# Performance work log

Measured on AMD Instinct MI355X. Metric: run time of the kernel, lower is better.

The kernel has to match this reference:

```python
import jax, jax.numpy as jnp
import numpy as np

N_GRAPHS = 32
NODES_PER_GRAPH = 512
N = N_GRAPHS * NODES_PER_GRAPH
DEG = 32
E = N * DEG
D = 128
HID = 256
NEXP = 8
EHID = 64
L = 3
CUTOFF = 10.0
ROUTE_W = 0.1


def _graph_norm(x, seg, w, b, ms, num, eps=1e-5):
    # PyG GraphNorm: x - mean_scale*mean_per_graph, normalized by per-graph std
    cnt = jax.ops.segment_sum(jnp.ones((x.shape[0],), x.dtype), seg, num_segments=num)[:, None]
    mean = jax.ops.segment_sum(x, seg, num_segments=num) / cnt
    out = x - ms * mean[seg]
    var = jax.ops.segment_sum(out * out, seg, num_segments=num) / cnt
    std = jnp.sqrt(var + eps)
    return w * out / std[seg] + b


def setup_inputs() -> dict:
    key = jax.random.key(0)
    ks = jax.random.split(key, 8)
    rng = np.random.default_rng(0)
    # radius-graph surrogate: each node gathers DEG in-graph neighbors
    tgt = np.repeat(np.arange(N), DEG)
    src = (tgt // NODES_PER_GRAPH) * NODES_PER_GRAPH + rng.integers(0, NODES_PER_GRAPH, size=E)
    edge_index = jnp.asarray(np.stack([src, tgt]), dtype=jnp.int32)
    batch = jnp.asarray(np.arange(N) // NODES_PER_GRAPH, dtype=jnp.int32)
    atom_type = jax.random.randint(ks[0], (N,), 0, 200, dtype=jnp.int32)
    pos = jax.random.uniform(ks[1], (N, 3), jnp.float32) * 5.0  # box side 5 -> dist < CUTOFF
    s = 0.1
    emb = jax.random.normal(ks[2], (200, D), jnp.float32) * s
    edge_w1 = jax.random.normal(ks[3], (L, 1, EHID), jnp.float32) * s
    edge_b1 = jnp.zeros((L, EHID), jnp.float32)
    edge_w2 = jax.random.normal(ks[4], (L, EHID, NEXP), jnp.float32) * s
    edge_b2 = jnp.zeros((L, NEXP), jnp.float32)
    node_w1 = jax.random.normal(ks[5], (L, NEXP, D, HID), jnp.float32) * s
    node_b1 = jnp.zeros((L, NEXP, HID), jnp.float32)
    node_w2 = jax.random.normal(ks[6], (L, NEXP, HID, D), jnp.float32) * s
    node_b2 = jnp.zeros((L, NEXP, D), jnp.float32)
    gn_w = jnp.ones((L, D), jnp.float32)
    gn_b = jnp.zeros((L, D), jnp.float32)
    gn_ms = jnp.ones((L, D), jnp.float32)
    dn_w = jnp.ones((1,), jnp.float32)
    dn_b = jnp.zeros((1,), jnp.float32)
    dn_ms = jnp.ones((1,), jnp.float32)
    return dict(pos=pos, emb=emb, edge_w1=edge_w1, edge_b1=edge_b1, edge_w2=edge_w2, edge_b2=edge_b2,
                node_w1=node_w1, node_b1=node_b1, node_w2=node_w2, node_b2=node_b2,
                gn_w=gn_w, gn_b=gn_b, gn_ms=gn_ms, dn_w=dn_w, dn_b=dn_b, dn_ms=dn_ms,
                atom_type=atom_type, edge_index=edge_index, batch=batch)


def reference(pos, emb, edge_w1, edge_b1, edge_w2, edge_b2, node_w1, node_b1, node_w2, node_b2,
              gn_w, gn_b, gn_ms, dn_w, dn_b, dn_ms, atom_type, edge_index, batch):
    src, dst = edge_index[0], edge_index[1]  # message j -> i
    dist = jnp.sqrt(jnp.sum((pos[src] - pos[dst]) ** 2, axis=-1))  # [E]
    ebatch = batch[src]
    edge_attr0 = _graph_norm(dist[:, None], ebatch, dn_w, dn_b, dn_ms, N_GRAPHS)  # [E,1]
    ew = (CUTOFF - dist[:, None]) / CUTOFF  # [E,1]
    h = emb[atom_type]  # [N,D]
    total_lbl = jnp.float32(0.0)
    for l in range(L):
        hid_e = jnp.maximum(edge_attr0 @ edge_w1[l] + edge_b1[l], 0.0)  # [E,EHID]
        ea = jax.nn.softmax(hid_e @ edge_w2[l] + edge_b2[l], axis=-1)  # [E,NEXP]
        total_lbl = total_lbl + jnp.sum(jnp.mean(ea, axis=0) ** 2) * NEXP / L
        eaw = ea * ew  # [E,NEXP] routing weight * distance weight
        x_j = h[src]  # [E,D] gathered once per layer
        out = jnp.zeros((N, D), h.dtype)
        for e in range(NEXP):
            agg = jax.ops.segment_sum(x_j * eaw[:, e:e + 1], dst, num_segments=N)  # [N,D]
            h2 = jnp.maximum(agg @ node_w1[l, e] + node_b1[l, e], 0.0) @ node_w2[l, e] + node_b2[l, e]
            out = out + h2
        h = out
        if l + 1 < L:
            h = jnp.tanh(_graph_norm(h, batch, gn_w[l], gn_b[l], gn_ms[l], N_GRAPHS))
    cnt = jax.ops.segment_sum(jnp.ones((N,), h.dtype), batch, num_segments=N_GRAPHS)[:, None]
    pooled = (jax.ops.segment_sum(h, batch, num_segments=N_GRAPHS) / cnt).mean(-1)  # [G]
    return pooled, total_lbl * ROUTE_W
```

## Files before the change

kernel.cpp:

```cpp
#include <hip/hip_runtime.h>
#include <math.h>

#define NG    32
#define NPG   512
#define NN    16384
#define DEG   32
#define NE    524288
#define EPG   16384
#define DD    128
#define HIDN  256
#define NEXPT 8
#define EHID  64
#define NL    3

typedef __attribute__((ext_vector_type(8))) short bh8;
typedef __attribute__((ext_vector_type(4))) float f4;

__device__ __forceinline__ unsigned short bf16_1(float x) {
  unsigned int u = __float_as_uint(x);
  return (unsigned short)((u + 0x7fffu + ((u >> 16) & 1u)) >> 16);
}
__device__ __forceinline__ unsigned int bf16pair(float a, float b) {
  return (unsigned int)bf16_1(a) | ((unsigned int)bf16_1(b) << 16);
}

__global__ void k_zero(float4* p, int n4) {
  int i = blockIdx.x * 256 + threadIdx.x;
  if (i < n4) p[i] = make_float4(0.f, 0.f, 0.f, 0.f);
}

__global__ void k_tr(const float* __restrict__ in, unsigned short* __restrict__ outp,
                     int M, int N) {
  __shared__ float tile[32][33];
  const float* ip = in + (size_t)blockIdx.z * M * N;
  unsigned short* op = outp + (size_t)blockIdx.z * M * N;
  int t = threadIdx.x;
  int i = t >> 5, j = t & 31;
  int c0 = blockIdx.x * 32, r0 = blockIdx.y * 32;
#pragma unroll
  for (int p = 0; p < 4; ++p)
    tile[i + 8 * p][j] = ip[(size_t)(r0 + i + 8 * p) * N + c0 + j];
  __syncthreads();
#pragma unroll
  for (int p = 0; p < 4; ++p)
    op[(size_t)(c0 + i + 8 * p) * M + r0 + j] = bf16_1(tile[j][i + 8 * p]);
}

__global__ void k_dist(const float* __restrict__ pos, const int* __restrict__ src,
                       const int* __restrict__ dst, float* __restrict__ dist,
                       float* __restrict__ gsum, float* __restrict__ gsq) {
  int e = blockIdx.x * 256 + threadIdx.x;
  int s = src[e], t = dst[e];
  float dx = pos[3 * s]     - pos[3 * t];
  float dy = pos[3 * s + 1] - pos[3 * t + 1];
  float dz = pos[3 * s + 2] - pos[3 * t + 2];
  float d = sqrtf(dx * dx + dy * dy + dz * dz);
  dist[e] = d;
  float s1 = d, s2 = d * d;
  for (int o = 32; o; o >>= 1) { s1 += __shfl_down(s1, o); s2 += __shfl_down(s2, o); }
  __shared__ float r1[4], r2[4];
  int w = threadIdx.x >> 6;
  if ((threadIdx.x & 63) == 0) { r1[w] = s1; r2[w] = s2; }
  __syncthreads();
  if (threadIdx.x == 0) {
    int g = e >> 14;
    atomicAdd(&gsum[g], r1[0] + r1[1] + r1[2] + r1[3]);
    atomicAdd(&gsq[g],  r2[0] + r2[1] + r2[2] + r2[3]);
  }
}

__global__ void k_efin(const float* __restrict__ gsum, const float* __restrict__ gsq,
                       const float* __restrict__ dnw, const float* __restrict__ dnb,
                       const float* __restrict__ dnms, float* __restrict__ ga, float* __restrict__ gb) {
  int g = threadIdx.x;
  if (g < NG) {
    float ms = dnms[0];
    float mean = gsum[g] * (1.f / EPG);
    float var = gsq[g] * (1.f / EPG) - (2.f * ms - ms * ms) * mean * mean;
    float a = dnw[0] * rsqrtf(var + 1e-5f);
    ga[g] = a;
    gb[g] = dnb[0] - a * ms * mean;
  }
}

__global__ void k_embed(const float4* __restrict__ emb, const int* __restrict__ at,
                        float4* __restrict__ h) {
  int gid = blockIdx.x * 256 + threadIdx.x;
  int i = gid >> 5, q = gid & 31;
  h[gid] = emb[at[i] * 32 + q];
}

__global__ void k_edge(const float* __restrict__ dist,
                       const float* __restrict__ ga, const float* __restrict__ gb,
                       const float* __restrict__ ew1, const float* __restrict__ eb1,
                       const float* __restrict__ ew2, const float* __restrict__ eb2,
                       float* __restrict__ eaw, float* __restrict__ part) {
  __shared__ float w1s[EHID], b1s[EHID];
  __shared__ __align__(16) float w2s[EHID * NEXPT];
  __shared__ float b2s[NEXPT];
  int t = threadIdx.x;
  if (t < EHID) { w1s[t] = ew1[t]; b1s[t] = eb1[t]; }
  if (t < NEXPT) b2s[t] = eb2[t];
  for (int j = t; j < EHID * NEXPT; j += 256) w2s[j] = ew2[j];
  __syncthreads();

  int e0 = blockIdx.x * 1024 + t * 4;
  float4 dv = *(const float4*)&dist[e0];
  float dd[4] = {dv.x, dv.y, dv.z, dv.w};
  int g = e0 >> 14;
  float gav = ga[g], gbv = gb[g];
  float a0[4], ewv[4];
#pragma unroll
  for (int j = 0; j < 4; ++j) {
    a0[j] = gav * dd[j] + gbv;
    ewv[j] = (10.0f - dd[j]) * 0.1f;
  }
  float acc[4][NEXPT];
#pragma unroll
  for (int j = 0; j < 4; ++j)
#pragma unroll
    for (int x = 0; x < NEXPT; ++x) acc[j][x] = b2s[x];

  for (int k = 0; k < EHID; ++k) {
    float w1k = w1s[k], b1k = b1s[k];
    float hk[4];
#pragma unroll
    for (int j = 0; j < 4; ++j) hk[j] = fmaxf(a0[j] * w1k + b1k, 0.f);
    float4 wa = *(const float4*)&w2s[k * 8];
    float4 wb = *(const float4*)&w2s[k * 8 + 4];
    float ww[8] = {wa.x, wa.y, wa.z, wa.w, wb.x, wb.y, wb.z, wb.w};
#pragma unroll
    for (int j = 0; j < 4; ++j)
#pragma unroll
      for (int x = 0; x < NEXPT; ++x) acc[j][x] += hk[j] * ww[x];
  }

  float esum[NEXPT] = {0, 0, 0, 0, 0, 0, 0, 0};
#pragma unroll
  for (int j = 0; j < 4; ++j) {
    float m = acc[j][0];
#pragma unroll
    for (int x = 1; x < NEXPT; ++x) m = fmaxf(m, acc[j][x]);
    float p[NEXPT], s = 0.f;
#pragma unroll
    for (int x = 0; x < NEXPT; ++x) { p[x] = __expf(acc[j][x] - m); s += p[x]; }
    float inv = 1.f / s;
    float fw = ewv[j] * inv;
    float4 o0 = {p[0] * fw, p[1] * fw, p[2] * fw, p[3] * fw};
    float4 o1 = {p[4] * fw, p[5] * fw, p[6] * fw, p[7] * fw};
    *(float4*)&eaw[(size_t)(e0 + j) * 8]     = o0;
    *(float4*)&eaw[(size_t)(e0 + j) * 8 + 4] = o1;
#pragma unroll
    for (int x = 0; x < NEXPT; ++x) esum[x] += p[x] * inv;
  }
  for (int o = 32; o; o >>= 1)
#pragma unroll
    for (int x = 0; x < NEXPT; ++x) esum[x] += __shfl_down(esum[x], o);
  __shared__ float ps[4][NEXPT];
  int w = t >> 6;
  if ((t & 63) == 0)
#pragma unroll
    for (int x = 0; x < NEXPT; ++x) ps[w][x] = esum[x];
  __syncthreads();
  if (t < NEXPT) part[blockIdx.x * NEXPT + t] = ps[0][t] + ps[1][t] + ps[2][t] + ps[3][t];
}

__global__ __launch_bounds__(256) void k_agg(const float* __restrict__ h, const int* __restrict__ src,
                      const float* __restrict__ eaw, unsigned short* __restrict__ agg) {
  const int t = threadIdx.x;
  const int s = t >> 5;
  const int lane = t & 31;
  const int i = blockIdx.x * 8 + s;
  __shared__ int ssrc[8][DEG];
  __shared__ __align__(16) float sw[8][DEG][NEXPT];
  const int e0b = blockIdx.x * 8 * DEG;
  ssrc[s][lane] = src[e0b + t];
  {
    const float4* ep = (const float4*)&eaw[(size_t)e0b * 8];
    float4* sp = (float4*)&sw[0][0][0];
    sp[t] = ep[t];
    sp[t + 256] = ep[t + 256];
  }
  __syncthreads();
  f4 acc[NEXPT];
#pragma unroll
  for (int x = 0; x < NEXPT; ++x) acc[x] = (f4)0.f;
#pragma unroll 2
  for (int k = 0; k < DEG; ++k) {
    f4 hv = *(const f4*)&h[(size_t)ssrc[s][k] * 128 + lane * 4];
    f4 w0 = *(const f4*)&sw[s][k][0];
    f4 w1 = *(const f4*)&sw[s][k][4];
    float ww[8] = {w0[0], w0[1], w0[2], w0[3], w1[0], w1[1], w1[2], w1[3]};
#pragma unroll
    for (int x = 0; x < NEXPT; ++x) acc[x] += ww[x] * hv;
  }
#pragma unroll
  for (int x = 0; x < NEXPT; ++x) {
    uint2 pk;
    pk.x = bf16pair(acc[x][0], acc[x][1]);
    pk.y = bf16pair(acc[x][2], acc[x][3]);
    *(uint2*)&agg[((size_t)x * NN + i) * 128 + lane * 4] = pk;
  }
}

__global__ __launch_bounds__(256) void k_mlp(
    const unsigned short* __restrict__ agg,
    const unsigned short* __restrict__ w1t,
    const float* __restrict__ b1g,
    const unsigned short* __restrict__ w2t,
    float* __restrict__ part) {
  __shared__ unsigned short hid[2][64 * 256];
  char* hb = (char*)hid;
  const int t = threadIdx.x;
  const int w = t >> 6;
  const int l15 = t & 15;
  const int q = (t & 63) >> 4;
  const int i0 = blockIdx.x * 64;
  const int x0 = blockIdx.y * 4;
  float* pout = part + (size_t)blockIdx.y * NN * 128;

  f4 acc2[2][4];
#pragma unroll
  for (int dt = 0; dt < 2; ++dt)
#pragma unroll
    for (int nt = 0; nt < 4; ++nt) acc2[dt][nt] = (f4)0.f;

  for (int xi = 0; xi < 4; ++xi) {
    const int x = x0 + xi;
    const int bufb = (xi & 1) * 32768;
    f4 acc1[4][4];
#pragma unroll
    for (int ht = 0; ht < 4; ++ht) {
      f4 bb = *(const f4*)&b1g[x * 256 + 64 * w + 16 * ht + 4 * q];
#pragma unroll
      for (int nt = 0; nt < 4; ++nt) acc1[ht][nt] = bb;
    }
#pragma unroll
    for (int ks = 0; ks < 4; ++ks) {
      bh8 afr[4], bfr[4];
#pragma unroll
      for (int ht = 0; ht < 4; ++ht)
        afr[ht] = *(const bh8*)&w1t[((size_t)x * 256 + 64 * w + 16 * ht + l15) * 128 + ks * 32 + q * 8];
#pragma unroll
      for (int nt = 0; nt < 4; ++nt)
        bfr[nt] = *(const bh8*)&agg[((size_t)x * NN + i0 + 16 * nt + l15) * 128 + ks * 32 + q * 8];
#pragma unroll
      for (int ht = 0; ht < 4; ++ht)
#pragma unroll
        for (int nt = 0; nt < 4; ++nt)
          acc1[ht][nt] = __builtin_amdgcn_mfma_f32_16x16x32_bf16(afr[ht], bfr[nt], acc1[ht][nt], 0, 0, 0);
    }
#pragma unroll
    for (int ht = 0; ht < 4; ++ht)
#pragma unroll
      for (int nt = 0; nt < 4; ++nt) {
        int node = 16 * nt + l15;
        int h0 = 64 * w + 16 * ht + 4 * q;
        int byte0 = bufb + ((node * 512 + h0 * 2) ^ ((node & 7) << 4));
        *(unsigned int*)(hb + byte0) =
            bf16pair(fmaxf(acc1[ht][nt][0], 0.f), fmaxf(acc1[ht][nt][1], 0.f));
        *(unsigned int*)(hb + byte0 + 4) =
            bf16pair(fmaxf(acc1[ht][nt][2], 0.f), fmaxf(acc1[ht][nt][3], 0.f));
      }
    __syncthreads();
#pragma unroll
    for (int ks = 0; ks < 8; ++ks) {
      bh8 a2[2], b2f[4];
#pragma unroll
      for (int dt = 0; dt < 2; ++dt)
        a2[dt] = *(const bh8*)&w2t[((size_t)x * 128 + 32 * w + 16 * dt + l15) * 256 + ks * 32 + q * 8];
#pragma unroll
      for (int nt = 0; nt < 4; ++nt) {
        int node = 16 * nt + l15;
        int byte0 = bufb + ((node * 512 + ks * 64 + q * 16) ^ ((node & 7) << 4));
        b2f[nt] = *(const bh8*)(hb + byte0);
      }
#pragma unroll
      for (int dt = 0; dt < 2; ++dt)
#pragma unroll
        for (int nt = 0; nt < 4; ++nt)
          acc2[dt][nt] = __builtin_amdgcn_mfma_f32_16x16x32_bf16(a2[dt], b2f[nt], acc2[dt][nt], 0, 0, 0);
    }
  }
#pragma unroll
  for (int dt = 0; dt < 2; ++dt)
#pragma unroll
    for (int nt = 0; nt < 4; ++nt)
      *(f4*)&pout[(size_t)(i0 + 16 * nt + l15) * 128 + 32 * w + 16 * dt + 4 * q] = acc2[dt][nt];
}

__global__ void k_red(const float4* __restrict__ part, float4* __restrict__ outp,
                      const float* __restrict__ b2g) {
  int i = blockIdx.x * 256 + threadIdx.x;
  int d4 = i & 31;
  float4 b = make_float4(0.f, 0.f, 0.f, 0.f);
#pragma unroll
  for (int x = 0; x < NEXPT; ++x) {
    float4 bv = *(const float4*)&b2g[x * 128 + d4 * 4];
    b.x += bv.x; b.y += bv.y; b.z += bv.z; b.w += bv.w;
  }
  float4 a0 = part[i];
  float4 a1 = part[i + NN * 128 / 4];
  float4 r = {a0.x + a1.x + b.x, a0.y + a1.y + b.y, a0.z + a1.z + b.z, a0.w + a1.w + b.w};
  outp[i] = r;
}

__global__ void k_gnr(const float* __restrict__ h, float* __restrict__ nsum, float* __restrict__ nsq) {
  int g = blockIdx.x, strip = blockIdx.y;
  int c = threadIdx.x;
  const float* base = h + ((size_t)g * NPG + strip * 64) * 128 + c;
  float s = 0.f, q = 0.f;
  for (int n = 0; n < 64; ++n) { float v = base[(size_t)n * 128]; s += v; q += v * v; }
  atomicAdd(&nsum[g * 128 + c], s);
  atomicAdd(&nsq[g * 128 + c], q);
}

__global__ void k_gnf(const float* __restrict__ nsum, const float* __restrict__ nsq,
                      const float* __restrict__ gw, const float* __restrict__ gbv,
                      const float* __restrict__ gms, float* __restrict__ amul, float* __restrict__ aadd) {
  int idx = blockIdx.x * 256 + threadIdx.x;
  int c = idx & 127;
  float ms = gms[c];
  float mean = nsum[idx] * (1.f / NPG);
  float var = nsq[idx] * (1.f / NPG) - (2.f * ms - ms * ms) * mean * mean;
  float a = gw[c] * rsqrtf(var + 1e-5f);
  amul[idx] = a;
  aadd[idx] = gbv[c] - a * ms * mean;
}

__global__ void k_gna(float* __restrict__ h, const float* __restrict__ amul,
                      const float* __restrict__ aadd) {
  int gid = blockIdx.x * 256 + threadIdx.x;
  int i = gid >> 5, q = gid & 31;
  int g = i >> 9;
  float4 v = *(float4*)&h[(size_t)gid * 4];
  float4 a = *(const float4*)&amul[g * 128 + q * 4];
  float4 b = *(const float4*)&aadd[g * 128 + q * 4];
  v.x = tanhf(a.x * v.x + b.x);
  v.y = tanhf(a.y * v.y + b.y);
  v.z = tanhf(a.z * v.z + b.z);
  v.w = tanhf(a.w * v.w + b.w);
  *(float4*)&h[(size_t)gid * 4] = v;
}

__global__ void k_pool(const float* __restrict__ h, float* __restrict__ outp) {
  int g = blockIdx.x, t = threadIdx.x;
  const float4* base = (const float4*)(h + (size_t)g * NPG * 128);
  float s = 0.f;
  for (int p = 0; p < 64; ++p) { float4 v = base[p * 256 + t]; s += v.x + v.y + v.z + v.w; }
  for (int o = 32; o; o >>= 1) s += __shfl_down(s, o);
  __shared__ float r[4];
  if ((t & 63) == 0) r[t >> 6] = s;
  __syncthreads();
  if (t == 0) outp[g] = (r[0] + r[1] + r[2] + r[3]) * (1.f / (NPG * 128));
}

__global__ void k_lbl(const float* __restrict__ part, float* __restrict__ outp) {
  __shared__ float s[NL * NEXPT];
  int t = threadIdx.x;
  if (t < NL * NEXPT) {
    int l = t >> 3, x = t & 7;
    float acc = 0.f;
    for (int b = 0; b < 512; ++b) acc += part[(size_t)(l * 512 + b) * NEXPT + x];
    s[t] = acc;
  }
  __syncthreads();
  if (t == 0) {
    float lbl = 0.f;
    for (int j = 0; j < NL * NEXPT; ++j) { float m = s[j] * (1.f / NE); lbl += m * m; }
    outp[0] = lbl * ((float)NEXPT / NL) * 0.1f;
  }
}

extern "C" void kernel_launch(void* const* d_in, const int* in_sizes, int n_in,
                              void* d_out, int out_size, void* d_ws, size_t ws_size,
                              hipStream_t stream) {
  (void)in_sizes; (void)n_in; (void)out_size; (void)ws_size;
  const float* pos  = (const float*)d_in[0];
  const float* emb  = (const float*)d_in[1];
  const float* ew1  = (const float*)d_in[2];
  const float* eb1  = (const float*)d_in[3];
  const float* ew2  = (const float*)d_in[4];
  const float* eb2  = (const float*)d_in[5];
  const float* nw1  = (const float*)d_in[6];
  const float* nb1  = (const float*)d_in[7];
  const float* nw2  = (const float*)d_in[8];
  const float* nb2  = (const float*)d_in[9];
  const float* gnw  = (const float*)d_in[10];
  const float* gnb  = (const float*)d_in[11];
  const float* gnms = (const float*)d_in[12];
  const float* dnw  = (const float*)d_in[13];
  const float* dnb  = (const float*)d_in[14];
  const float* dnms = (const float*)d_in[15];
  const int* atom   = (const int*)d_in[16];
  const int* eidx   = (const int*)d_in[17];
  float* out = (float*)d_out;

  char* wsb = (char*)d_ws;
  float* dist = (float*)wsb;                 wsb += sizeof(float) * NE;
  float* eaw  = (float*)wsb;                 wsb += sizeof(float) * (size_t)NE * 8;
  unsigned short* aggb = (unsigned short*)wsb; wsb += sizeof(short) * (size_t)8 * NN * 128;
  unsigned short* w1t  = (unsigned short*)wsb; wsb += sizeof(short) * (size_t)NL * 8 * 256 * 128;
  unsigned short* w2t  = (unsigned short*)wsb; wsb += sizeof(short) * (size_t)NL * 8 * 256 * 128;
  float* hA   = (float*)wsb;                 wsb += sizeof(float) * (size_t)NN * 128;
  float* hB   = (float*)wsb;                 wsb += sizeof(float) * (size_t)NN * 128;
  float* gsum = (float*)wsb;                 wsb += sizeof(float) * NG;
  float* gsq  = (float*)wsb;                 wsb += sizeof(float) * NG;
  float* ga   = (float*)wsb;                 wsb += sizeof(float) * NG;
  float* gb   = (float*)wsb;                 wsb += sizeof(float) * NG;
  float* nsum = (float*)wsb;                 wsb += sizeof(float) * NG * 128;
  float* nsq  = (float*)wsb;                 wsb += sizeof(float) * NG * 128;
  float* amul = (float*)wsb;                 wsb += sizeof(float) * NG * 128;
  float* aadd = (float*)wsb;                 wsb += sizeof(float) * NG * 128;
  float* part = (float*)wsb;                 wsb += sizeof(float) * (size_t)NL * 512 * NEXPT;

  float* mpart = eaw;

  const int* srcA = eidx;
  const int* dstA = eidx + NE;

  k_zero<<<1, 256, 0, stream>>>((float4*)gsum, 16);
  {
    dim3 g1(HIDN / 32, DD / 32, NL * NEXPT);
    k_tr<<<g1, 256, 0, stream>>>(nw1, w1t, DD, HIDN);
    dim3 g2(DD / 32, HIDN / 32, NL * NEXPT);
    k_tr<<<g2, 256, 0, stream>>>(nw2, w2t, HIDN, DD);
  }
  k_dist<<<NE / 256, 256, 0, stream>>>(pos, srcA, dstA, dist, gsum, gsq);
  k_efin<<<1, 64, 0, stream>>>(gsum, gsq, dnw, dnb, dnms, ga, gb);
  k_embed<<<NN * 32 / 256, 256, 0, stream>>>((const float4*)emb, atom, (float4*)hA);

  float* hcur = hA;
  float* hnxt = hB;
  for (int l = 0; l < NL; ++l) {
    k_edge<<<NE / 1024, 256, 0, stream>>>(dist, ga, gb, ew1 + l * EHID, eb1 + l * EHID,
                                          ew2 + (size_t)l * EHID * NEXPT, eb2 + l * NEXPT,
                                          eaw, part + (size_t)l * 512 * NEXPT);
    k_agg<<<NN / 8, 256, 0, stream>>>(hcur, srcA, eaw, aggb);
    {
      dim3 gm(NN / 64, 2);
      k_mlp<<<gm, 256, 0, stream>>>(aggb,
                                    w1t + (size_t)l * 8 * 256 * 128,
                                    nb1 + (size_t)l * 8 * 256,
                                    w2t + (size_t)l * 8 * 256 * 128,
                                    mpart);
    }
    k_red<<<NN * 128 / 4 / 256, 256, 0, stream>>>((const float4*)mpart, (float4*)hnxt,
                                                  nb2 + (size_t)l * 8 * 128);
    if (l + 1 < NL) {
      k_zero<<<8, 256, 0, stream>>>((float4*)nsum, 2048);
      dim3 gr(NG, 8);
      k_gnr<<<gr, 128, 0, stream>>>(hnxt, nsum, nsq);
      k_gnf<<<16, 256, 0, stream>>>(nsum, nsq, gnw + l * 128, gnb + l * 128, gnms + l * 128,
                                    amul, aadd);
      k_gna<<<NN * 32 / 256, 256, 0, stream>>>(hnxt, amul, aadd);
    }
    float* tmp = hcur; hcur = hnxt; hnxt = tmp;
  }
  k_pool<<<NG, 256, 0, stream>>>(hcur, out);
  k_lbl<<<1, 64, 0, stream>>>(part, out + NG);
}
```

Before: 492.7 us.

## Fuse edge routing into aggregation and pre-swizzle MFMA operand layouts

Merges the edge-MLP/softmax kernel with the neighbor aggregation kernel so routing weights stay in shared memory instead of making a round trip through a global eaw buffer. The aggregated features and both expert weight matrices are written in a fragment-ordered layout so k_mlp loads each MFMA operand as one contiguous 16-byte chunk per lane. The graph-norm finalize kernel is folded into the apply kernel. The fused kernel uses about 40KB of shared memory and runs only 512 blocks, each processing 32 nodes serially, which may lower occupancy and latency hiding for the gather.

```diff
diff --git a/kernel.cpp b/kernel.cpp
--- a/kernel.cpp
+++ b/kernel.cpp
@@ -29,21 +29,38 @@
   if (i < n4) p[i] = make_float4(0.f, 0.f, 0.f, 0.f);
 }
 
-__global__ void k_tr(const float* __restrict__ in, unsigned short* __restrict__ outp,
-                     int M, int N) {
-  __shared__ float tile[32][33];
-  const float* ip = in + (size_t)blockIdx.z * M * N;
-  unsigned short* op = outp + (size_t)blockIdx.z * M * N;
-  int t = threadIdx.x;
-  int i = t >> 5, j = t & 31;
-  int c0 = blockIdx.x * 32, r0 = blockIdx.y * 32;
-#pragma unroll
-  for (int p = 0; p < 4; ++p)
-    tile[i + 8 * p][j] = ip[(size_t)(r0 + i + 8 * p) * N + c0 + j];
-  __syncthreads();
-#pragma unroll
-  for (int p = 0; p < 4; ++p)
-    op[(size_t)(c0 + i + 8 * p) * M + r0 + j] = bf16_1(tile[j][i + 8 * p]);
+__global__ void k_trf1(const float* __restrict__ in, unsigned short* __restrict__ outp) {
+  int c = blockIdx.x * 256 + threadIdx.x;
+  int le = c >> 12, hblk = (c >> 8) & 15, ks = (c >> 6) & 3, l = c & 63;
+  int l15 = l & 15, q = l >> 4;
+  const float* base = in + (size_t)le * 32768;
+  unsigned short v[8];
+#pragma unroll
+  for (int j = 0; j < 8; ++j)
+    v[j] = bf16_1(base[(ks * 32 + q * 8 + j) * 256 + hblk * 16 + l15]);
+  uint4 pk;
+  pk.x = (unsigned)v[0] | ((unsigned)v[1] << 16);
+  pk.y = (unsigned)v[2] | ((unsigned)v[3] << 16);
+  pk.z = (unsigned)v[4] | ((unsigned)v[5] << 16);
+  pk.w = (unsigned)v[6] | ((unsigned)v[7] << 16);
+  *(uint4*)&outp[(size_t)c * 8] = pk;
+}
+
+__global__ void k_trf2(const float* __restrict__ in, unsigned short* __restrict__ outp) {
+  int c = blockIdx.x * 256 + threadIdx.x;
+  int le = c >> 12, dblk = (c >> 9) & 7, ksh = (c >> 6) & 7, l = c & 63;
+  int l15 = l & 15, q = l >> 4;
+  const float* base = in + (size_t)le * 32768;
+  unsigned short v[8];
+#pragma unroll
+  for (int j = 0; j < 8; ++j)
+    v[j] = bf16_1(base[(ksh * 32 + q * 8 + j) * 128 + dblk * 16 + l15]);
+  uint4 pk;
+  pk.x = (unsigned)v[0] | ((unsigned)v[1] << 16);
+  pk.y = (unsigned)v[2] | ((unsigned)v[3] << 16);
+  pk.z = (unsigned)v[4] | ((unsigned)v[5] << 16);
+  pk.w = (unsigned)v[6] | ((unsigned)v[7] << 16);
+  *(uint4*)&outp[(size_t)c * 8] = pk;
 }
 
 __global__ void k_dist(const float* __restrict__ pos, const int* __restrict__ src,
@@ -90,21 +107,28 @@
   h[gid] = emb[at[i] * 32 + q];
 }
 
-__global__ void k_edge(const float* __restrict__ dist,
-                       const float* __restrict__ ga, const float* __restrict__ gb,
-                       const float* __restrict__ ew1, const float* __restrict__ eb1,
-                       const float* __restrict__ ew2, const float* __restrict__ eb2,
-                       float* __restrict__ eaw, float* __restrict__ part) {
+__global__ __launch_bounds__(256) void k_ea(
+    const float* __restrict__ dist, const float* __restrict__ ga, const float* __restrict__ gb,
+    const float* __restrict__ ew1, const float* __restrict__ eb1,
+    const float* __restrict__ ew2, const float* __restrict__ eb2,
+    const float* __restrict__ h, const int* __restrict__ src,
+    unsigned short* __restrict__ aggf, float* __restrict__ part) {
   __shared__ float w1s[EHID], b1s[EHID];
   __shared__ __align__(16) float w2s[EHID * NEXPT];
   __shared__ float b2s[NEXPT];
+  __shared__ __align__(16) float sw[1024][NEXPT];
+  __shared__ int ssrc[1024];
+  __shared__ float ps[4][NEXPT];
   int t = threadIdx.x;
   if (t < EHID) { w1s[t] = ew1[t]; b1s[t] = eb1[t]; }
   if (t < NEXPT) b2s[t] = eb2[t];
   for (int j = t; j < EHID * NEXPT; j += 256) w2s[j] = ew2[j];
+  const int e0b = blockIdx.x * 1024;
+#pragma unroll
+  for (int k = 0; k < 4; ++k) ssrc[t + 256 * k] = src[e0b + t + 256 * k];
   __syncthreads();
 
-  int e0 = blockIdx.x * 1024 + t * 4;
+  int e0 = e0b + t * 4;
   float4 dv = *(const float4*)&dist[e0];
   float dd[4] = {dv.x, dv.y, dv.z, dv.w};
   int g = e0 >> 14;
@@ -120,7 +144,6 @@
   for (int j = 0; j < 4; ++j)
 #pragma unroll
     for (int x = 0; x < NEXPT; ++x) acc[j][x] = b2s[x];
-
   for (int k = 0; k < EHID; ++k) {
     float w1k = w1s[k], b1k = b1s[k];
     float hk[4];
@@ -134,7 +157,6 @@
 #pragma unroll
       for (int x = 0; x < NEXPT; ++x) acc[j][x] += hk[j] * ww[x];
   }
-
   float esum[NEXPT] = {0, 0, 0, 0, 0, 0, 0, 0};
 #pragma unroll
   for (int j = 0; j < 4; ++j) {
@@ -148,74 +170,63 @@
     float fw = ewv[j] * inv;
     float4 o0 = {p[0] * fw, p[1] * fw, p[2] * fw, p[3] * fw};
     float4 o1 = {p[4] * fw, p[5] * fw, p[6] * fw, p[7] * fw};
-    *(float4*)&eaw[(size_t)(e0 + j) * 8]     = o0;
-    *(float4*)&eaw[(size_t)(e0 + j) * 8 + 4] = o1;
+    *(float4*)&sw[t * 4 + j][0] = o0;
+    *(float4*)&sw[t * 4 + j][4] = o1;
 #pragma unroll
     for (int x = 0; x < NEXPT; ++x) esum[x] += p[x] * inv;
   }
   for (int o = 32; o; o >>= 1)
 #pragma unroll
     for (int x = 0; x < NEXPT; ++x) esum[x] += __shfl_down(esum[x], o);
-  __shared__ float ps[4][NEXPT];
-  int w = t >> 6;
+  int wv = t >> 6;
   if ((t & 63) == 0)
 #pragma unroll
-    for (int x = 0; x < NEXPT; ++x) ps[w][x] = esum[x];
+    for (int x = 0; x < NEXPT; ++x) ps[wv][x] = esum[x];
   __syncthreads();
   if (t < NEXPT) part[blockIdx.x * NEXPT + t] = ps[0][t] + ps[1][t] + ps[2][t] + ps[3][t];
-}
-
-__global__ __launch_bounds__(256) void k_agg(const float* __restrict__ h, const int* __restrict__ src,
-                      const float* __restrict__ eaw, unsigned short* __restrict__ agg) {
-  const int t = threadIdx.x;
-  const int s = t >> 5;
-  const int lane = t & 31;
-  const int i = blockIdx.x * 8 + s;
-  __shared__ int ssrc[8][DEG];
-  __shared__ __align__(16) float sw[8][DEG][NEXPT];
-  const int e0b = blockIdx.x * 8 * DEG;
-  ssrc[s][lane] = src[e0b + t];
-  {
-    const float4* ep = (const float4*)&eaw[(size_t)e0b * 8];
-    float4* sp = (float4*)&sw[0][0][0];
-    sp[t] = ep[t];
-    sp[t + 256] = ep[t + 256];
-  }
-  __syncthreads();
-  f4 acc[NEXPT];
-#pragma unroll
-  for (int x = 0; x < NEXPT; ++x) acc[x] = (f4)0.f;
+
+  const int s8 = t >> 5, lane = t & 31;
+  for (int oct = 0; oct < 4; ++oct) {
+    int iloc = oct * 8 + s8;
+    int i = blockIdx.x * 32 + iloc;
+    f4 ac[NEXPT];
+#pragma unroll
+    for (int x = 0; x < NEXPT; ++x) ac[x] = (f4)0.f;
 #pragma unroll 2
-  for (int k = 0; k < DEG; ++k) {
-    f4 hv = *(const f4*)&h[(size_t)ssrc[s][k] * 128 + lane * 4];
-    f4 w0 = *(const f4*)&sw[s][k][0];
-    f4 w1 = *(const f4*)&sw[s][k][4];
-    float ww[8] = {w0[0], w0[1], w0[2], w0[3], w1[0], w1[1], w1[2], w1[3]};
-#pragma unroll
-    for (int x = 0; x < NEXPT; ++x) acc[x] += ww[x] * hv;
-  }
-#pragma unroll
-  for (int x = 0; x < NEXPT; ++x) {
-    uint2 pk;
-    pk.x = bf16pair(acc[x][0], acc[x][1]);
-    pk.y = bf16pair(acc[x][2], acc[x][3]);
-    *(uint2*)&agg[((size_t)x * NN + i) * 128 + lane * 4] = pk;
+    for (int k = 0; k < DEG; ++k) {
+      f4 hv = *(const f4*)&h[(size_t)ssrc[iloc * 32 + k] * 128 + lane * 4];
+      f4 w0 = *(const f4*)&sw[iloc * 32 + k][0];
+      f4 w1v = *(const f4*)&sw[iloc * 32 + k][4];
+      float ww[8] = {w0[0], w0[1], w0[2], w0[3], w1v[0], w1v[1], w1v[2], w1v[3]};
+#pragma unroll
+      for (int x = 0; x < NEXPT; ++x) ac[x] += ww[x] * hv;
+    }
+#pragma unroll
+    for (int x = 0; x < NEXPT; ++x) {
+      uint2 pk;
+      pk.x = bf16pair(ac[x][0], ac[x][1]);
+      pk.y = bf16pair(ac[x][2], ac[x][3]);
+      size_t off = ((((size_t)x * 1024 + (i >> 4)) * 4 + (lane >> 3)) * 64 +
+                    ((i & 15) + 16 * ((lane >> 1) & 3))) * 16 + (lane & 1) * 8;
+      *(uint2*)((char*)aggf + off) = pk;
+    }
   }
 }
 
 __global__ __launch_bounds__(256) void k_mlp(
-    const unsigned short* __restrict__ agg,
-    const unsigned short* __restrict__ w1t,
+    const unsigned short* __restrict__ aggf,
+    const unsigned short* __restrict__ w1tf,
     const float* __restrict__ b1g,
-    const unsigned short* __restrict__ w2t,
+    const unsigned short* __restrict__ w2tf,
     float* __restrict__ part) {
   __shared__ unsigned short hid[2][64 * 256];
   char* hb = (char*)hid;
   const int t = threadIdx.x;
-  const int w = t >> 6;
+  const int w = t >> 6, t63 = t & 63;
   const int l15 = t & 15;
   const int q = (t & 63) >> 4;
-  const int i0 = blockIdx.x * 64;
+  const int bx = blockIdx.x;
+  const int i0 = bx * 64;
   const int x0 = blockIdx.y * 4;
   float* pout = part + (size_t)blockIdx.y * NN * 128;
 
@@ -240,10 +251,10 @@
       bh8 afr[4], bfr[4];
 #pragma unroll
       for (int ht = 0; ht < 4; ++ht)
-        afr[ht] = *(const bh8*)&w1t[((size_t)x * 256 + 64 * w + 16 * ht + l15) * 128 + ks * 32 + q * 8];
+        afr[ht] = *(const bh8*)&w1tf[((((size_t)x * 16 + 4 * w + ht) * 4 + ks) * 64 + t63) * 8];
 #pragma unroll
       for (int nt = 0; nt < 4; ++nt)
-        bfr[nt] = *(const bh8*)&agg[((size_t)x * NN + i0 + 16 * nt + l15) * 128 + ks * 32 + q * 8];
+        bfr[nt] = *(const bh8*)&aggf[((((size_t)x * 1024 + bx * 4 + nt) * 4 + ks) * 64 + t63) * 8];
 #pragma unroll
       for (int ht = 0; ht < 4; ++ht)
 #pragma unroll
@@ -268,7 +279,7 @@
       bh8 a2[2], b2f[4];
 #pragma unroll
       for (int dt = 0; dt < 2; ++dt)
-        a2[dt] = *(const bh8*)&w2t[((size_t)x * 128 + 32 * w + 16 * dt + l15) * 256 + ks * 32 + q * 8];
+        a2[dt] = *(const bh8*)&w2tf[((((size_t)x * 8 + 2 * w + dt) * 8 + ks) * 64 + t63) * 8];
 #pragma unroll
       for (int nt = 0; nt < 4; ++nt) {
         int node = 16 * nt + l15;
@@ -315,31 +326,34 @@
   atomicAdd(&nsq[g * 128 + c], q);
 }
 
-__global__ void k_gnf(const float* __restrict__ nsum, const float* __restrict__ nsq,
-                      const float* __restrict__ gw, const float* __restrict__ gbv,
-                      const float* __restrict__ gms, float* __restrict__ amul, float* __restrict__ aadd) {
-  int idx = blockIdx.x * 256 + threadIdx.x;
-  int c = idx & 127;
-  float ms = gms[c];
-  float mean = nsum[idx] * (1.f / NPG);
-  float var = nsq[idx] * (1.f / NPG) - (2.f * ms - ms * ms) * mean * mean;
-  float a = gw[c] * rsqrtf(var + 1e-5f);
-  amul[idx] = a;
-  aadd[idx] = gbv[c] - a * ms * mean;
-}
-
-__global__ void k_gna(float* __restrict__ h, const float* __restrict__ amul,
-                      const float* __restrict__ aadd) {
+__global__ void k_gna(float* __restrict__ h, const float* __restrict__ nsum,
+                      const float* __restrict__ nsq, const float* __restrict__ gw,
+                      const float* __restrict__ gbv, const float* __restrict__ gms) {
   int gid = blockIdx.x * 256 + threadIdx.x;
   int i = gid >> 5, q = gid & 31;
   int g = i >> 9;
+  float4 s1 = *(const float4*)&nsum[g * 128 + q * 4];
+  float4 s2 = *(const float4*)&nsq[g * 128 + q * 4];
+  float4 msv = *(const float4*)&gms[q * 4];
+  float4 wvv = *(const float4*)&gw[q * 4];
+  float4 bvv = *(const float4*)&gbv[q * 4];
   float4 v = *(float4*)&h[(size_t)gid * 4];
-  float4 a = *(const float4*)&amul[g * 128 + q * 4];
-  float4 b = *(const float4*)&aadd[g * 128 + q * 4];
-  v.x = tanhf(a.x * v.x + b.x);
-  v.y = tanhf(a.y * v.y + b.y);
-  v.z = tanhf(a.z * v.z + b.z);
-  v.w = tanhf(a.w * v.w + b.w);
+  float sa[4] = {s1.x, s1.y, s1.z, s1.w};
+  float sq[4] = {s2.x, s2.y, s2.z, s2.w};
+  float mm[4] = {msv.x, msv.y, msv.z, msv.w};
+  float wa[4] = {wvv.x, wvv.y, wvv.z, wvv.w};
+  float ba[4] = {bvv.x, bvv.y, bvv.z, bvv.w};
+  float vv[4] = {v.x, v.y, v.z, v.w};
+#pragma unroll
+  for (int j = 0; j < 4; ++j) {
+    float ms = mm[j];
+    float mean = sa[j] * (1.f / NPG);
+    float var = sq[j] * (1.f / NPG) - (2.f * ms - ms * ms) * mean * mean;
+    float a = wa[j] * rsqrtf(var + 1e-5f);
+    float b = ba[j] - a * ms * mean;
+    vv[j] = tanhf(a * vv[j] + b);
+  }
+  v.x = vv[0]; v.y = vv[1]; v.z = vv[2]; v.w = vv[3];
   *(float4*)&h[(size_t)gid * 4] = v;
 }
 
@@ -397,35 +411,27 @@
   float* out = (float*)d_out;
 
   char* wsb = (char*)d_ws;
-  float* dist = (float*)wsb;                 wsb += sizeof(float) * NE;
-  float* eaw  = (float*)wsb;                 wsb += sizeof(float) * (size_t)NE * 8;
-  unsigned short* aggb = (unsigned short*)wsb; wsb += sizeof(short) * (size_t)8 * NN * 128;
-  unsigned short* w1t  = (unsigned short*)wsb; wsb += sizeof(short) * (size_t)NL * 8 * 256 * 128;
-  unsigned short* w2t  = (unsigned short*)wsb; wsb += sizeof(short) * (size_t)NL * 8 * 256 * 128;
-  float* hA   = (float*)wsb;                 wsb += sizeof(float) * (size_t)NN * 128;
-  float* hB   = (float*)wsb;                 wsb += sizeof(float) * (size_t)NN * 128;
-  float* gsum = (float*)wsb;                 wsb += sizeof(float) * NG;
-  float* gsq  = (float*)wsb;                 wsb += sizeof(float) * NG;
-  float* ga   = (float*)wsb;                 wsb += sizeof(float) * NG;
-  float* gb   = (float*)wsb;                 wsb += sizeof(float) * NG;
-  float* nsum = (float*)wsb;                 wsb += sizeof(float) * NG * 128;
-  float* nsq  = (float*)wsb;                 wsb += sizeof(float) * NG * 128;
-  float* amul = (float*)wsb;                 wsb += sizeof(float) * NG * 128;
-  float* aadd = (float*)wsb;                 wsb += sizeof(float) * NG * 128;
-  float* part = (float*)wsb;                 wsb += sizeof(float) * (size_t)NL * 512 * NEXPT;
-
-  float* mpart = eaw;
+  float* dist = (float*)wsb;                   wsb += sizeof(float) * NE;
+  float* mpart = (float*)wsb;                  wsb += sizeof(float) * (size_t)2 * NN * 128;
+  unsigned short* aggf = (unsigned short*)wsb; wsb += sizeof(short) * (size_t)8 * NN * 128;
+  unsigned short* w1tf = (unsigned short*)wsb; wsb += sizeof(short) * (size_t)NL * 8 * 256 * 128;
+  unsigned short* w2tf = (unsigned short*)wsb; wsb += sizeof(short) * (size_t)NL * 8 * 256 * 128;
+  float* hA   = (float*)wsb;                   wsb += sizeof(float) * (size_t)NN * 128;
+  float* hB   = (float*)wsb;                   wsb += sizeof(float) * (size_t)NN * 128;
+  float* gsum = (float*)wsb;                   wsb += sizeof(float) * NG;
+  float* gsq  = (float*)wsb;                   wsb += sizeof(float) * NG;
+  float* ga   = (float*)wsb;                   wsb += sizeof(float) * NG;
+  float* gb   = (float*)wsb;                   wsb += sizeof(float) * NG;
+  float* nsum = (float*)wsb;                   wsb += sizeof(float) * NG * 128;
+  float* nsq  = (float*)wsb;                   wsb += sizeof(float) * NG * 128;
+  float* part = (float*)wsb;                   wsb += sizeof(float) * (size_t)NL * 512 * NEXPT;
 
   const int* srcA = eidx;
   const int* dstA = eidx + NE;
 
   k_zero<<<1, 256, 0, stream>>>((float4*)gsum, 16);
-  {
-    dim3 g1(HIDN / 32, DD / 32, NL * NEXPT);
-    k_tr<<<g1, 256, 0, stream>>>(nw1, w1t, DD, HIDN);
-    dim3 g2(DD / 32, HIDN / 32, NL * NEXPT);
-    k_tr<<<g2, 256, 0, stream>>>(nw2, w2t, HIDN, DD);
-  }
+  k_trf1<<<384, 256, 0, stream>>>(nw1, w1tf);
+  k_trf2<<<384, 256, 0, stream>>>(nw2, w2tf);
   k_dist<<<NE / 256, 256, 0, stream>>>(pos, srcA, dstA, dist, gsum, gsq);
   k_efin<<<1, 64, 0, stream>>>(gsum, gsq, dnw, dnb, dnms, ga, gb);
   k_embed<<<NN * 32 / 256, 256, 0, stream>>>((const float4*)emb, atom, (float4*)hA);
@@ -433,16 +439,15 @@
   float* hcur = hA;
   float* hnxt = hB;
   for (int l = 0; l < NL; ++l) {
-    k_edge<<<NE / 1024, 256, 0, stream>>>(dist, ga, gb, ew1 + l * EHID, eb1 + l * EHID,
-                                          ew2 + (size_t)l * EHID * NEXPT, eb2 + l * NEXPT,
-                                          eaw, part + (size_t)l * 512 * NEXPT);
-    k_agg<<<NN / 8, 256, 0, stream>>>(hcur, srcA, eaw, aggb);
+    k_ea<<<NE / 1024, 256, 0, stream>>>(dist, ga, gb, ew1 + l * EHID, eb1 + l * EHID,
+                                        ew2 + (size_t)l * EHID * NEXPT, eb2 + l * NEXPT,
+                                        hcur, srcA, aggf, part + (size_t)l * 512 * NEXPT);
     {
       dim3 gm(NN / 64, 2);
-      k_mlp<<<gm, 256, 0, stream>>>(aggb,
-                                    w1t + (size_t)l * 8 * 256 * 128,
+      k_mlp<<<gm, 256, 0, stream>>>(aggf,
+                                    w1tf + (size_t)l * 262144,
                                     nb1 + (size_t)l * 8 * 256,
-                                    w2t + (size_t)l * 8 * 256 * 128,
+                                    w2tf + (size_t)l * 262144,
                                     mpart);
     }
     k_red<<<NN * 128 / 4 / 256, 256, 0, stream>>>((const float4*)mpart, (float4*)hnxt,
@@ -451,9 +456,8 @@
       k_zero<<<8, 256, 0, stream>>>((float4*)nsum, 2048);
       dim3 gr(NG, 8);
       k_gnr<<<gr, 128, 0, stream>>>(hnxt, nsum, nsq);
-      k_gnf<<<16, 256, 0, stream>>>(nsum, nsq, gnw + l * 128, gnb + l * 128, gnms + l * 128,
-                                    amul, aadd);
-      k_gna<<<NN * 32 / 256, 256, 0, stream>>>(hnxt, amul, aadd);
+      k_gna<<<NN * 32 / 256, 256, 0, stream>>>(hnxt, nsum, nsq,
+                                               gnw + l * 128, gnb + l * 128, gnms + l * 128);
     }
     float* tmp = hcur; hcur = hnxt; hnxt = tmp;
   }
```

After: 416.8 us. 15.4% less time.
